# Performance work log

Hardware: AMD Instinct MI355X
Metric: run time of the kernel (lower is better)

Reference implementation:

```python
import jax, jax.numpy as jnp
import numpy as np

B, TC, TT, E, V = 512, 64, 16, 512, 256
E2 = E // 2


def entmax15(z):
    # exact sort-based 1.5-entmax over last axis (Peters et al., 2019)
    z = z / 2.0
    z = z - jnp.max(z, axis=-1, keepdims=True)  # shift-invariant, for stability
    z_srt = -jnp.sort(-z, axis=-1)
    d = z.shape[-1]
    rho = jnp.arange(1, d + 1, dtype=z.dtype)
    mean = jnp.cumsum(z_srt, axis=-1) / rho
    mean_sq = jnp.cumsum(z_srt * z_srt, axis=-1) / rho
    ss = rho * (mean_sq - mean * mean)
    delta = (1.0 - ss) / rho
    pos = delta > 0
    sqrt_d = jnp.where(pos, jnp.sqrt(jnp.where(pos, delta, 1.0)), 0.0)
    tau = mean - sqrt_d
    k = jnp.sum((tau <= z_srt).astype(jnp.int32), axis=-1, keepdims=True)
    tau_star = jnp.take_along_axis(tau, k - 1, axis=-1)
    y = jnp.clip(z - tau_star, 0.0)
    return y * y


def _mha(q_seq, kv, wq, wk, wv, bq, bk, bv, wo, bo):
    # single-head attention; q_seq: (T,B,E) decoder states, kv: (B,S,E) encoder memory
    e = q_seq.shape[-1]
    q = (q_seq @ wq.T + bq) * (1.0 / jnp.sqrt(jnp.asarray(e, q_seq.dtype)))
    k = kv @ wk.T + bk
    v = kv @ wv.T + bv
    a = jax.nn.softmax(jnp.einsum('tbe,bse->bts', q, k), axis=-1)
    o = jnp.einsum('bts,bse->tbe', a, v)
    return o @ wo.T + bo


def setup_inputs() -> dict:
    key = jax.random.key(0)
    ks = jax.random.split(key, 20)
    rn = lambda k, s, sc=1.0: sc * jax.random.normal(k, s, dtype=jnp.float32)
    z = lambda s: jnp.zeros(s, jnp.float32)
    return {
        'char_encoding': rn(ks[0], (B, TC, E)),
        'char_hn0': rn(ks[1], (B, E2)),
        'char_cn0': rn(ks[2], (B, E2)),
        'tag_encoding': rn(ks[3], (B, TT, E)),
        'tag_hn0': rn(ks[4], (B, E2)),
        'tag_cn0': rn(ks[5], (B, E2)),
        'true_output_seq': jax.random.uniform(ks[6], (B, TC, V), dtype=jnp.float32),
        'w_ih': rn(ks[7], (4 * E, V), 0.05),
        'w_hh': rn(ks[8], (4 * E, E), 0.05),
        'b_ih': z((4 * E,)),
        'b_hh': z((4 * E,)),
        'char_wq': rn(ks[9], (E, E), 0.05), 'char_wk': rn(ks[10], (E, E), 0.05), 'char_wv': rn(ks[11], (E, E), 0.05),
        'char_bq': z((E,)), 'char_bk': z((E,)), 'char_bv': z((E,)),
        'char_wo': rn(ks[12], (E, E), 0.05), 'char_bo': z((E,)),
        'tag_wq': rn(ks[13], (E, E), 0.05), 'tag_wk': rn(ks[14], (E, E), 0.05), 'tag_wv': rn(ks[15], (E, E), 0.05),
        'tag_bq': z((E,)), 'tag_bk': z((E,)), 'tag_bv': z((E,)),
        'tag_wo': rn(ks[16], (E, E), 0.05), 'tag_bo': z((E,)),
        'out_w': rn(ks[17], (V, 2 * E), 0.05),
        'out_b': z((V,)),
    }


def reference(char_encoding, char_hn0, char_cn0, tag_encoding, tag_hn0, tag_cn0, true_output_seq, w_ih, w_hh, b_ih, b_hh, char_wq, char_wk, char_wv, char_bq, char_bk, char_bv, char_wo, char_bo, tag_wq, tag_wk, tag_wv, tag_bq, tag_bk, tag_bv, tag_wo, tag_bo, out_w, out_b):
    # initial cell state = concat of the two encoders' final (h, c)
    h0 = jnp.concatenate([char_hn0, tag_hn0], axis=-1)
    c0 = jnp.concatenate([char_cn0, tag_cn0], axis=-1)
    # teacher forcing: input at t=0 is zeros, then true_output_seq[:, t]
    xs = jnp.concatenate([jnp.zeros_like(true_output_seq[:, :1]), true_output_seq[:, 1:]], axis=1)
    xs = jnp.swapaxes(xs, 0, 1)  # (T, B, V)

    def cell(carry, x):
        h, c = carry
        gates = x @ w_ih.T + b_ih + h @ w_hh.T + b_hh
        i, f, g, o = jnp.split(gates, 4, axis=-1)  # torch gate order i,f,g,o
        c = jax.nn.sigmoid(f) * c + jax.nn.sigmoid(i) * jnp.tanh(g)
        h = jax.nn.sigmoid(o) * jnp.tanh(c)
        return (h, c), h

    _, hs = jax.lax.scan(cell, (h0, c0), xs)  # (T, B, E)
    # attention queries only depend on per-step h, so batch all T queries at once
    ca = _mha(hs, char_encoding, char_wq, char_wk, char_wv, char_bq, char_bk, char_bv, char_wo, char_bo)
    ta = _mha(hs, tag_encoding, tag_wq, tag_wk, tag_wv, tag_bq, tag_bk, tag_bv, tag_wo, tag_bo)
    logits = jnp.concatenate([ca, ta], axis=-1) @ out_w.T + out_b  # (T, B, V)
    return jnp.swapaxes(entmax15(logits), 0, 1)  # (B, T, V)
```

## Files before the change

kernel.cpp:

```cpp
#include <hip/hip_runtime.h>

typedef unsigned short us;
typedef unsigned int u32;
typedef unsigned long long u64;
typedef __bf16 bf16x8 __attribute__((ext_vector_type(8)));
typedef float f32x4 __attribute__((ext_vector_type(4)));

#define MFMA(a,b,c) __builtin_amdgcn_mfma_f32_16x16x32_bf16(a,b,c,0,0,0)

__device__ __forceinline__ us f2bf(float f){
  u32 u = __builtin_bit_cast(u32, f);
  u += 0x7fffu + ((u>>16)&1u);
  return (us)(u>>16);
}
__device__ __forceinline__ float bf2f(us h){
  u32 u = ((u32)h)<<16;
  return __builtin_bit_cast(float, u);
}
__device__ __forceinline__ float sigf(float x){ return 1.0f/(1.0f+__expf(-x)); }
__device__ __forceinline__ float tanh_(float x){ float e=__expf(2.0f*x); return 1.0f - 2.0f/(e+1.0f); }


__global__ void k_prep_wperm(const float* __restrict__ w_hh, const float* __restrict__ w_ih,
                             const float* __restrict__ b_ih, const float* __restrict__ b_hh,
                             us* __restrict__ Wp, float* __restrict__ biasc){
  int n = blockIdx.x; int c = threadIdx.x;
  float v = (c < 512) ? w_hh[(size_t)n*512 + c] : w_ih[(size_t)n*256 + (c-512)];
  int g = n >> 9, eg = n & 511, eb = eg >> 4, ln = eg & 15;
  int kc = c >> 5, qd = (c >> 3) & 3, i = c & 7;
  size_t dst = ((((size_t)eb*24 + kc)*4 + g)*64 + (size_t)(qd*16 + ln))*8 + i;
  Wp[dst] = f2bf(v);
  if (c == 0) biasc[n] = b_ih[n] + b_hh[n];
}

__global__ void k_prep_state(const float* __restrict__ ch, const float* __restrict__ th,
                             const float* __restrict__ cc, const float* __restrict__ tc,
                             us* __restrict__ h0, float* __restrict__ c0){
  int i = blockIdx.x*256 + threadIdx.x;
  int b = i>>9, e = i&511;
  float hv = (e<256)? ch[b*256+e] : th[b*256+e-256];
  float cv = (e<256)? cc[b*256+e] : tc[b*256+e-256];
  h0[i] = f2bf(hv); c0[i] = cv;
}

__global__ void k_xprep(const float* __restrict__ x, us* __restrict__ xbf){
  int g = blockIdx.x*256 + threadIdx.x;
  int v0 = (g & 31) * 8;
  int b  = (g >> 5) & 511;
  int t  = g >> 14;
  const float4* src = (const float4*)(x + ((size_t)(b*64 + t))*256 + v0);
  float4 f0 = src[0], f1 = src[1];
  uint4 pk;
  pk.x = (u32)f2bf(f0.x) | ((u32)f2bf(f0.y)<<16);
  pk.y = (u32)f2bf(f0.z) | ((u32)f2bf(f0.w)<<16);
  pk.z = (u32)f2bf(f1.x) | ((u32)f2bf(f1.y)<<16);
  pk.w = (u32)f2bf(f1.z) | ((u32)f2bf(f1.w)<<16);
  *(uint4*)(xbf + ((size_t)t*512 + b)*256 + v0) = pk;
}

__global__ void k_uvec2(const float* __restrict__ bq, const float* __restrict__ wk,
                        float* __restrict__ u){
  int j = blockIdx.x*256 + threadIdx.x;
  int e0 = blockIdx.y*64;
  float a = 0.f;
  #pragma unroll 8
  for (int e=e0; e<e0+64; ++e) a += bq[e]*wk[(size_t)e*512 + j];
  atomicAdd(u+j, a);
}

__global__ __launch_bounds__(256) void k_pvec2(const float* __restrict__ wo,
    const float* __restrict__ bv, const float* __restrict__ bo, float* __restrict__ p){
  int w = threadIdx.x>>6, lane = threadIdx.x&63;
  int i = blockIdx.x*4 + w;
  const float4* wr = (const float4*)(wo + (size_t)i*512);
  const float4* bvv = (const float4*)bv;
  float a = 0.f;
  #pragma unroll
  for (int k=0;k<2;++k){
    float4 x = wr[lane*2+k];
    float4 y = bvv[lane*2+k];
    a += x.x*y.x + x.y*y.y + x.z*y.z + x.w*y.w;
  }
  #pragma unroll
  for (int dl=1; dl<64; dl<<=1) a += __shfl_xor(a, dl);
  if (lane==0) p[i] = a + bo[i];
}

__global__ __launch_bounds__(256) void k_bc2(const float* __restrict__ out_w,
    const float* __restrict__ pc, const float* __restrict__ pt,
    const float* __restrict__ out_b, float* __restrict__ bc){
  int w = threadIdx.x>>6, lane = threadIdx.x&63;
  int v = blockIdx.x*4 + w;
  const float4* wr = (const float4*)(out_w + (size_t)v*1024);
  float a = 0.f;
  #pragma unroll
  for (int k=0;k<4;++k){
    float4 x = wr[lane*4+k];
    int base = (lane*4+k)*4;
    const float* pv = (base < 512) ? (pc + base) : (pt + (base-512));
    a += x.x*pv[0] + x.y*pv[1] + x.z*pv[2] + x.w*pv[3];
  }
  #pragma unroll
  for (int dl=1; dl<64; dl<<=1) a += __shfl_xor(a, dl);
  if (lane==0) bc[v] = a + out_b[v];
}

template<bool TA, int OMODE>
__global__ __launch_bounds__(256) void k_pgemm(const float* __restrict__ A, int lda,
    const float* __restrict__ B, int ldb, void* C1, void* C2, int ldc, int K){
  __shared__ us As[64][40];
  __shared__ us Bs[64][40];
  int tid=threadIdx.x, w=tid>>6, lane=tid&63, qd=lane>>4, ln=lane&15;
  int m0 = blockIdx.x*64, n0 = blockIdx.y*64;
  f32x4 acc[4] = {};
  for (int kc=0; kc<K/32; ++kc){
    int k0 = kc*32;
    if (!TA){
      int r=tid>>2, c=(tid&3)*8;
      const float* ap = A + (size_t)(m0+r)*lda + k0 + c;
      float4 f0=*(const float4*)ap, f1=*(const float4*)(ap+4);
      uint4 pk;
      pk.x=(u32)f2bf(f0.x)|((u32)f2bf(f0.y)<<16);
      pk.y=(u32)f2bf(f0.z)|((u32)f2bf(f0.w)<<16);
      pk.z=(u32)f2bf(f1.x)|((u32)f2bf(f1.y)<<16);
      pk.w=(u32)f2bf(f1.z)|((u32)f2bf(f1.w)<<16);
      *(uint4*)&As[r][c] = pk;
    } else {
      int kk=tid>>3, mp=(tid&7)*8;
      const float* ap = A + (size_t)(k0+kk)*lda + m0 + mp;
      #pragma unroll
      for (int i=0;i<8;++i) As[mp+i][kk] = f2bf(ap[i]);
    }
    { int kk=tid>>3, np=(tid&7)*8;
      const float* bp = B + (size_t)(k0+kk)*ldb + n0 + np;
      #pragma unroll
      for (int i=0;i<8;++i) Bs[np+i][kk] = f2bf(bp[i]);
    }
    __syncthreads();
    bf16x8 a = *(const bf16x8*)&As[16*w+ln][qd*8];
    #pragma unroll
    for (int j=0;j<4;++j){
      bf16x8 bb = *(const bf16x8*)&Bs[16*j+ln][qd*8];
      acc[j] = MFMA(a, bb, acc[j]);
    }
    __syncthreads();
  }
  #pragma unroll
  for (int j=0;j<4;++j){
    #pragma unroll
    for (int r=0;r<4;++r){
      size_t idx = (size_t)(m0+16*w+qd*4+r)*ldc + (n0+16*j+ln);
      float v = acc[j][r];
      if (OMODE==0) ((float*)C1)[idx] = v;
      else if (OMODE==1) ((us*)C1)[idx] = f2bf(v);
      else {
        us h = f2bf(v);
        ((us*)C1)[idx] = h;
        ((us*)C2)[idx] = f2bf(v - bf2f(h));
      }
    }
  }
}

__global__ __launch_bounds__(256, 1) void k_lstm_all(
    const us* __restrict__ h0, const us* __restrict__ xbf,
    const us* __restrict__ Wp, const float* __restrict__ biasc,
    const float* __restrict__ c0, us* __restrict__ hs,
    unsigned* __restrict__ bars){
  extern __shared__ us Wf[];
  int tid = threadIdx.x, w = tid>>6, lane = tid&63, qd = lane>>4, ln = lane&15;
  int bb = blockIdx.x & 7, eb = blockIdx.x >> 3;
  int b0 = bb*64, e0 = eb*16;

  u32 myxcc = 0;
  asm volatile("s_getreg_b32 %0, hwreg(HW_REG_XCC_ID)" : "=s"(myxcc));
  unsigned* xcds = bars + 4096 + (size_t)bb*512;
  if (tid == 0)
    __hip_atomic_store(xcds + eb*16, myxcc + 1u, __ATOMIC_RELAXED, __HIP_MEMORY_SCOPE_AGENT);

  {
    const uint4* src = (const uint4*)(Wp + (size_t)eb*49152);
    uint4* dst = (uint4*)Wf;
    #pragma unroll
    for (int i=0;i<24;++i) dst[tid + 256*i] = src[tid + 256*i];
  }
  int bA = b0 + 16*w + ln;
  int bC = b0 + 16*w + qd*4;
  int e  = e0 + ln;
  float bias_[4], c_[4];
  #pragma unroll
  for (int j=0;j<4;++j) bias_[j] = biasc[j*512 + e];
  #pragma unroll
  for (int r=0;r<4;++r) c_[r] = c0[(size_t)(bC+r)*512 + e];
  __syncthreads();

  bool fast;
  {
    const unsigned* xp = xcds + (lane&31)*16;
    u32 ids;
    while (true){
      ids = __hip_atomic_load(xp, __ATOMIC_RELAXED, __HIP_MEMORY_SCOPE_AGENT);
      if (__all((int)(ids != 0))) break;
      __builtin_amdgcn_s_sleep(8);
    }
    u32 id0 = (u32)__shfl((int)ids, 0);
    fast = __all((int)(ids == id0));
  }

  unsigned* flags = bars + (size_t)bb*512;
  unsigned* myflag = flags + eb*16;
  const unsigned* pollp = flags + (lane&31)*16;
  f32x4 xacc[4] = {};
  for (int t=0; t<64; ++t){
    if (t > 0){
      unsigned tgt = (unsigned)t;
      while (true){
        unsigned v = __hip_atomic_load(pollp, __ATOMIC_RELAXED, __HIP_MEMORY_SCOPE_AGENT);
        if (__all((int)(v >= tgt))) break;
        __builtin_amdgcn_s_sleep(1);
      }
      asm volatile("" ::: "memory");
    }
    bf16x8 afr[16];
    if (t == 0){
      const us* hrow = h0 + (size_t)bA*512;
      #pragma unroll
      for (int kc=0; kc<16; ++kc)
        afr[kc] = *(const bf16x8*)(hrow + kc*32 + qd*8);
    } else if (fast){
      const us* hrow = hs + ((size_t)bA*64 + (t-1))*512;
      #pragma unroll
      for (int kc=0; kc<16; ++kc)
        afr[kc] = *(const bf16x8*)(hrow + kc*32 + qd*8);
    } else {
      const u64* hq = (const u64*)(hs + ((size_t)bA*64 + (t-1))*512);
      u64 q0[16], q1[16];
      #pragma unroll
      for (int kc=0; kc<16; ++kc){
        q0[kc] = __hip_atomic_load(hq + kc*8 + qd*2 + 0, __ATOMIC_RELAXED, __HIP_MEMORY_SCOPE_AGENT);
        q1[kc] = __hip_atomic_load(hq + kc*8 + qd*2 + 1, __ATOMIC_RELAXED, __HIP_MEMORY_SCOPE_AGENT);
      }
      #pragma unroll
      for (int kc=0; kc<16; ++kc){
        union { u64 q[2]; bf16x8 v; } u_;
        u_.q[0] = q0[kc]; u_.q[1] = q1[kc];
        afr[kc] = u_.v;
      }
    }
    f32x4 acc[4] = {xacc[0], xacc[1], xacc[2], xacc[3]};
    #pragma unroll
    for (int kc=0; kc<16; ++kc){
      #pragma unroll
      for (int j=0;j<4;++j){
        bf16x8 bfrag = *(const bf16x8*)&Wf[(size_t)((kc*4+j)*64 + lane)*8];
        acc[j] = MFMA(afr[kc], bfrag, acc[j]);
      }
    }
    us hb[4];
    #pragma unroll
    for (int r=0;r<4;++r){
      float iv = acc[0][r]+bias_[0], fv = acc[1][r]+bias_[1];
      float gv = acc[2][r]+bias_[2], ov = acc[3][r]+bias_[3];
      float cc2 = sigf(fv)*c_[r] + sigf(iv)*tanh_(gv);
      c_[r] = cc2;
      hb[r] = f2bf(sigf(ov)*tanh_(cc2));
    }
    #pragma unroll
    for (int r=0;r<4;++r){
      u32 v = hb[r];
      u32 p = v | (((u32)__shfl_xor((int)v, 1)) << 16);
      u64 q = (u64)p | (((u64)(u32)__shfl_xor((int)p, 2)) << 32);
      if ((lane & 3) == 0){
        size_t idx = ((size_t)(bC+r)*64 + t)*512 + e0 + ln;
        if (fast)
          *(u64*)(hs + idx) = q;
        else
          __hip_atomic_store((u64*)(hs + idx), q, __ATOMIC_RELAXED, __HIP_MEMORY_SCOPE_AGENT);
      }
    }
    if (t < 63){
      __syncthreads();
      if (tid == 0)
        __hip_atomic_store(myflag, (unsigned)(t+1), __ATOMIC_RELAXED, __HIP_MEMORY_SCOPE_AGENT);
      const us* xrow = xbf + ((size_t)(t+1)*512 + bA)*256;
      f32x4 xa[4] = {};
      #pragma unroll
      for (int kx=0; kx<8; ++kx){
        bf16x8 xf = *(const bf16x8*)(xrow + kx*32 + qd*8);
        #pragma unroll
        for (int j=0;j<4;++j){
          bf16x8 bfrag = *(const bf16x8*)&Wf[(size_t)(((16+kx)*4+j)*64 + lane)*8];
          xa[j] = MFMA(xf, bfrag, xa[j]);
        }
      }
      #pragma unroll
      for (int j=0;j<4;++j) xacc[j] = xa[j];
    }
  }
}

__global__ __launch_bounds__(256) void k_gemm(
    const us* __restrict__ Ap, const us* __restrict__ W,
    const float* __restrict__ bias, float alpha, us* __restrict__ C){
  __shared__ us As[128][40];
  __shared__ us Ws[128][40];
  int tid = threadIdx.x; int w = tid>>6; int lane=tid&63;
  int qd=lane>>4, ln=lane&15;
  int m0 = blockIdx.x*128, n0 = blockIdx.y*128;
  int wm = (w&1)*64, wn=(w>>1)*64;
  f32x4 acc[4][4] = {};
  int row = tid>>1; int cp = (tid&1)*16;
  for (int kc=0;kc<16;++kc){
    int k0=kc*32;
    { const uint4* ap = (const uint4*)(Ap + (size_t)(m0+row)*512 + k0+cp);
      *(uint4*)&As[row][cp]=ap[0]; *(uint4*)&As[row][cp+8]=ap[1];
    }
    { const uint4* wp = (const uint4*)(W + (size_t)(n0+row)*512 + k0+cp);
      *(uint4*)&Ws[row][cp]=wp[0]; *(uint4*)&Ws[row][cp+8]=wp[1];
    }
    __syncthreads();
    bf16x8 af[4], bfr[4];
    #pragma unroll
    for (int i=0;i<4;++i) af[i]  = *(const bf16x8*)&As[wm+16*i+ln][qd*8];
    #pragma unroll
    for (int j=0;j<4;++j) bfr[j] = *(const bf16x8*)&Ws[wn+16*j+ln][qd*8];
    #pragma unroll
    for (int i=0;i<4;++i)
      #pragma unroll
      for (int j=0;j<4;++j) acc[i][j]=MFMA(af[i],bfr[j],acc[i][j]);
    __syncthreads();
  }
  #pragma unroll
  for (int j=0;j<4;++j){
    int col = n0+wn+16*j+ln;
    float bv = bias[col];
    #pragma unroll
    for (int i=0;i<4;++i){
      #pragma unroll
      for (int r=0;r<4;++r){
        int rm = m0+wm+16*i+qd*4+r;
        C[(size_t)rm*512 + col] = f2bf(alpha*(acc[i][j][r]+bv));
      }
    }
  }
}

template<int S>
struct alignas(16) ASmem3 {
  static constexpr int SP  = (S<32)?32:S;
  static constexpr int SPp = SP+8;
  us Pbh[64][SPp];
  us Pbl[64][SPp];
  union {
    us Es[S][72];
    struct { us Eh[64][72]; us El[64][72]; } t;
  } u;
  us Ph[64][72];
  us Pl[64][72];
};

template<int S, bool ACC>
__global__ __launch_bounds__(256) void k_attn3(const us* __restrict__ hGp,
    const float* __restrict__ enc, const us* __restrict__ Mvh,
    const us* __restrict__ Mvl, float* __restrict__ out){
  constexpr int NJ  = S/16;
  constexpr int KC2 = ((S<32)?32:S)/32;
  extern __shared__ char smraw[];
  ASmem3<S>& sm = *reinterpret_cast<ASmem3<S>*>(smraw);
  int b = blockIdx.x;
  int tid=threadIdx.x, w=tid>>6, lane=tid&63, qd=lane>>4, ln=lane&15;

  f32x4 sacc[NJ];
  #pragma unroll
  for (int j=0;j<NJ;++j) sacc[j] = (f32x4){0.f,0.f,0.f,0.f};
  const us* hrow = hGp + ((size_t)(b*64 + 16*w + ln))*512;
  for (int ec=0; ec<8; ++ec){
    int e0 = ec*64;
    { int s = tid>>2, ep=(tid&3)*16;
      if (S==64 || tid < 4*S){
        const float* ap = enc + ((size_t)b*S + s)*512 + e0 + ep;
        float4 f0=*(const float4*)ap, f1=*(const float4*)(ap+4);
        float4 f2=*(const float4*)(ap+8), f3=*(const float4*)(ap+12);
        float fv[16]={f0.x,f0.y,f0.z,f0.w,f1.x,f1.y,f1.z,f1.w,
                      f2.x,f2.y,f2.z,f2.w,f3.x,f3.y,f3.z,f3.w};
        u32 pk[8];
        #pragma unroll
        for (int i=0;i<8;++i)
          pk[i] = (u32)f2bf(fv[2*i]) | ((u32)f2bf(fv[2*i+1])<<16);
        uint4* d = (uint4*)&sm.u.Es[s][ep];
        d[0] = make_uint4(pk[0],pk[1],pk[2],pk[3]);
        d[1] = make_uint4(pk[4],pk[5],pk[6],pk[7]);
      }
    }
    __syncthreads();
    #pragma unroll
    for (int kcl=0;kcl<2;++kcl){
      bf16x8 a = *(const bf16x8*)(hrow + e0 + kcl*32 + qd*8);
      #pragma unroll
      for (int j=0;j<NJ;++j){
        bf16x8 bb = *(const bf16x8*)&sm.u.Es[16*j+ln][kcl*32+qd*8];
        sacc[j] = MFMA(a, bb, sacc[j]);
      }
    }
    __syncthreads();
  }

  #pragma unroll
  for (int r=0;r<4;++r){
    float m = sacc[0][r];
    #pragma unroll
    for (int j=1;j<NJ;++j) m = fmaxf(m, sacc[j][r]);
    #pragma unroll
    for (int dl=1; dl<16; dl<<=1) m = fmaxf(m, __shfl_xor(m, dl));
    float ssum = 0.f;
    #pragma unroll
    for (int j=0;j<NJ;++j){ float e_=__expf(sacc[j][r]-m); sacc[j][r]=e_; ssum+=e_; }
    #pragma unroll
    for (int dl=1; dl<16; dl<<=1) ssum += __shfl_xor(ssum, dl);
    float inv = 1.0f/ssum;
    int R = 16*w + qd*4 + r;
    #pragma unroll
    for (int j=0;j<NJ;++j){
      float pv = sacc[j][r]*inv;
      us h = f2bf(pv);
      sm.Pbh[R][16*j+ln] = h;
      sm.Pbl[R][16*j+ln] = f2bf(pv - bf2f(h));
    }
    if (S==16){ sm.Pbh[R][16+ln]=0; sm.Pbl[R][16+ln]=0; }
  }

  f32x4 Lacc[4][4] = {};
  for (int ec=0; ec<8; ++ec){
    int e0 = ec*64;
    { int s = tid>>2, ep=(tid&3)*16;
      if (S==64 || tid < 4*S){
        const float* ap = enc + ((size_t)b*S + s)*512 + e0 + ep;
        float4 f0=*(const float4*)ap, f1=*(const float4*)(ap+4);
        float4 f2=*(const float4*)(ap+8), f3=*(const float4*)(ap+12);
        float fv[16]={f0.x,f0.y,f0.z,f0.w,f1.x,f1.y,f1.z,f1.w,
                      f2.x,f2.y,f2.z,f2.w,f3.x,f3.y,f3.z,f3.w};
        #pragma unroll
        for (int i=0;i<16;++i){
          float v = fv[i]; us h = f2bf(v);
          sm.u.t.Eh[ep+i][s] = h;
          sm.u.t.El[ep+i][s] = f2bf(v - bf2f(h));
        }
      } else if (S==16 && tid < 128){
        int s2 = 16 + ((tid-64)>>2);
        #pragma unroll
        for (int i=0;i<16;++i){ sm.u.t.Eh[ep+i][s2]=0; sm.u.t.El[ep+i][s2]=0; }
      }
    }
    __syncthreads();
    f32x4 pacc[4] = {};
    #pragma unroll
    for (int kcl=0;kcl<KC2;++kcl){
      bf16x8 ah = *(const bf16x8*)&sm.Pbh[16*w+ln][kcl*32+qd*8];
      bf16x8 al = *(const bf16x8*)&sm.Pbl[16*w+ln][kcl*32+qd*8];
      #pragma unroll
      for (int j=0;j<4;++j){
        bf16x8 bh = *(const bf16x8*)&sm.u.t.Eh[16*j+ln][kcl*32+qd*8];
        bf16x8 bl = *(const bf16x8*)&sm.u.t.El[16*j+ln][kcl*32+qd*8];
        pacc[j] = MFMA(ah, bh, pacc[j]);
        pacc[j] = MFMA(ah, bl, pacc[j]);
        pacc[j] = MFMA(al, bh, pacc[j]);
      }
    }
    #pragma unroll
    for (int j=0;j<4;++j)
      #pragma unroll
      for (int r=0;r<4;++r){
        float v = pacc[j][r]; us h = f2bf(v);
        sm.Ph[16*w+qd*4+r][16*j+ln] = h;
        sm.Pl[16*w+qd*4+r][16*j+ln] = f2bf(v - bf2f(h));
      }
    __syncthreads();
    #pragma unroll
    for (int kcl=0;kcl<2;++kcl){
      bf16x8 ah[4], al[4];
      #pragma unroll
      for (int i=0;i<4;++i){
        ah[i] = *(const bf16x8*)&sm.Ph[16*i+ln][kcl*32+qd*8];
        al[i] = *(const bf16x8*)&sm.Pl[16*i+ln][kcl*32+qd*8];
      }
      #pragma unroll
      for (int j=0;j<4;++j){
        int v = 64*w + 16*j + ln;
        bf16x8 mh = *(const bf16x8*)(Mvh + (size_t)v*512 + e0 + kcl*32 + qd*8);
        bf16x8 ml = *(const bf16x8*)(Mvl + (size_t)v*512 + e0 + kcl*32 + qd*8);
        #pragma unroll
        for (int i=0;i<4;++i){
          Lacc[i][j] = MFMA(ah[i], mh, Lacc[i][j]);
          Lacc[i][j] = MFMA(ah[i], ml, Lacc[i][j]);
          Lacc[i][j] = MFMA(al[i], mh, Lacc[i][j]);
        }
      }
    }
  }
  #pragma unroll
  for (int i=0;i<4;++i){
    #pragma unroll
    for (int j=0;j<4;++j){
      int v = 64*w + 16*j + ln;
      #pragma unroll
      for (int r=0;r<4;++r){
        size_t addr = ((size_t)b*64 + 16*i + qd*4 + r)*256 + v;
        if (ACC) out[addr] += Lacc[i][j][r];
        else     out[addr]  = Lacc[i][j][r];
      }
    }
  }
}

__global__ __launch_bounds__(256) void k_entmax(float* __restrict__ out,
                                                const float* __restrict__ bc){
  int tid=threadIdx.x; int w=tid>>6; int lane=tid&63;
  float4 bcv = *(const float4*)(bc + lane*4);
  int base = blockIdx.x*16 + w*4;
  for (int i=0;i<4;++i){
    int row = base + i;
    float* rp = out + (size_t)row*256 + lane*4;
    float4 d = *(const float4*)rp;
    float z[4] = {0.5f*(d.x+bcv.x), 0.5f*(d.y+bcv.y), 0.5f*(d.z+bcv.z), 0.5f*(d.w+bcv.w)};
    float m = fmaxf(fmaxf(z[0],z[1]), fmaxf(z[2],z[3]));
    #pragma unroll
    for (int dl=1; dl<64; dl<<=1) m = fmaxf(m, __shfl_xor(m, dl));
    #pragma unroll
    for (int k=0;k<4;++k) z[k] -= m;
    float tau = -1.0f;
    for (int it=0; it<14; ++it){
      float s1=0.f, s2=0.f;
      #pragma unroll
      for (int k=0;k<4;++k){
        float dd = z[k]-tau; dd = fmaxf(dd, 0.f);
        s1 += dd; s2 += dd*dd;
      }
      #pragma unroll
      for (int dl=1; dl<64; dl<<=1){ s1 += __shfl_xor(s1, dl); s2 += __shfl_xor(s2, dl); }
      tau += (s2 - 1.0f) / (2.0f*fmaxf(s1, 1e-12f));
    }
    float4 y;
    { float dd;
      dd = fmaxf(z[0]-tau,0.f); y.x = dd*dd;
      dd = fmaxf(z[1]-tau,0.f); y.y = dd*dd;
      dd = fmaxf(z[2]-tau,0.f); y.z = dd*dd;
      dd = fmaxf(z[3]-tau,0.f); y.w = dd*dd;
    }
    *(float4*)rp = y;
  }
}


extern "C" void kernel_launch(void* const* d_in, const int* in_sizes, int n_in,
                              void* d_out, int out_size, void* d_ws, size_t ws_size,
                              hipStream_t stream){
  (void)in_sizes; (void)n_in; (void)out_size; (void)ws_size;
  const float* char_enc = (const float*)d_in[0];
  const float* char_hn0 = (const float*)d_in[1];
  const float* char_cn0 = (const float*)d_in[2];
  const float* tag_enc  = (const float*)d_in[3];
  const float* tag_hn0  = (const float*)d_in[4];
  const float* tag_cn0  = (const float*)d_in[5];
  const float* true_out = (const float*)d_in[6];
  const float* w_ih = (const float*)d_in[7];
  const float* w_hh = (const float*)d_in[8];
  const float* b_ih = (const float*)d_in[9];
  const float* b_hh = (const float*)d_in[10];
  const float* c_wq = (const float*)d_in[11];
  const float* c_wk = (const float*)d_in[12];
  const float* c_wv = (const float*)d_in[13];
  const float* c_bq = (const float*)d_in[14];
  const float* c_bv = (const float*)d_in[16];
  const float* c_wo = (const float*)d_in[17];
  const float* c_bo = (const float*)d_in[18];
  const float* t_wq = (const float*)d_in[19];
  const float* t_wk = (const float*)d_in[20];
  const float* t_wv = (const float*)d_in[21];
  const float* t_bq = (const float*)d_in[22];
  const float* t_bv = (const float*)d_in[24];
  const float* t_wo = (const float*)d_in[25];
  const float* t_bo = (const float*)d_in[26];
  const float* out_w = (const float*)d_in[27];
  const float* out_b = (const float*)d_in[28];
  float* out = (float*)d_out;

  char* base = (char*)d_ws;
  char* regA = base;
  us*    Wp    = (us*)   (regA + 0);
  float* biasc = (float*)(regA + 3145728);
  us*    h0    = (us*)   (regA + 3153920);
  float* cst   = (float*)(regA + 3678208);
  float* M1f   = (float*)(regA + 4726784);
  float* M2f   = (float*)(regA + 5251072);
  us*    xbf   = (us*)   (regA + 5775360);
  us*    hG    = (us*)   regA;
  char* regB = base + 33554432;
  us*    Gc_w  = (us*)(regB + 0);
  us*    Gt_w  = (us*)(regB + 524288);
  us*    M1vh  = (us*)(regB + 1048576);
  us*    M1vl  = (us*)(regB + 1310720);
  us*    M2vh  = (us*)(regB + 1572864);
  us*    M2vl  = (us*)(regB + 1835008);
  float* u_c   = (float*)(regB + 2097152);
  float* u_t   = (float*)(regB + 2099200);
  float* p_c   = (float*)(regB + 2101248);
  float* p_t   = (float*)(regB + 2103296);
  float* bc    = (float*)(regB + 2105344);
  us*    hs    = (us*)(base + 33554432 + 2106368);
  unsigned* bars = (unsigned*)(base + 33554432 + 2106368 + 33554432);

  static bool attr_done = false;
  if (!attr_done){
    hipFuncSetAttribute(reinterpret_cast<const void*>(&k_lstm_all),
                        hipFuncAttributeMaxDynamicSharedMemorySize, 131072);
    attr_done = true;
  }

  hipMemsetAsync(bars, 0, 32768, stream);
  hipMemsetAsync(u_c, 0, 4096, stream);
  k_prep_wperm<<<2048, 768, 0, stream>>>(w_hh, w_ih, b_ih, b_hh, Wp, biasc);
  k_prep_state<<<1024, 256, 0, stream>>>(char_hn0, tag_hn0, char_cn0, tag_cn0, h0, cst);
  k_xprep<<<4096, 256, 0, stream>>>(true_out, xbf);
  k_pgemm<true,1><<<dim3(8,8),256,0,stream>>>(c_wk, 512, c_wq, 512, Gc_w, nullptr, 512, 512);
  k_pgemm<true,1><<<dim3(8,8),256,0,stream>>>(t_wk, 512, t_wq, 512, Gt_w, nullptr, 512, 512);
  k_pgemm<false,0><<<dim3(4,8),256,0,stream>>>(out_w,     1024, c_wo, 512, M1f, nullptr, 512, 512);
  k_pgemm<false,0><<<dim3(4,8),256,0,stream>>>(out_w+512, 1024, t_wo, 512, M2f, nullptr, 512, 512);
  k_pgemm<false,2><<<dim3(4,8),256,0,stream>>>(M1f, 512, c_wv, 512, M1vh, M1vl, 512, 512);
  k_pgemm<false,2><<<dim3(4,8),256,0,stream>>>(M2f, 512, t_wv, 512, M2vh, M2vl, 512, 512);
  k_uvec2<<<dim3(2,8),256,0,stream>>>(c_bq, c_wk, u_c);
  k_uvec2<<<dim3(2,8),256,0,stream>>>(t_bq, t_wk, u_t);
  k_pvec2<<<128,256,0,stream>>>(c_wo, c_bv, c_bo, p_c);
  k_pvec2<<<128,256,0,stream>>>(t_wo, t_bv, t_bo, p_t);
  k_bc2<<<64,256,0,stream>>>(out_w, p_c, p_t, out_b, bc);

  k_lstm_all<<<256, 256, 98304, stream>>>(h0, xbf, Wp, biasc, cst, hs, bars);

  const float scale = 0.044194173824159216f;
  k_gemm<<<dim3(256,4),256,0,stream>>>(hs, Gc_w, u_c, scale, hG);
  k_attn3<64,false><<<512,256,sizeof(ASmem3<64>),stream>>>(hG, char_enc, M1vh, M1vl, out);
  k_gemm<<<dim3(256,4),256,0,stream>>>(hs, Gt_w, u_t, scale, hG);
  k_attn3<16,true ><<<512,256,sizeof(ASmem3<16>),stream>>>(hG, tag_enc, M2vh, M2vl, out);
  k_entmax<<<2048,256,0,stream>>>(out, bc);
}
```

Measured before the change: 963.7 us.

## Start LSTM recurrent MFMAs per ready h-chunk and batch paired weight-prep launches

In the persistent LSTM kernel's fast path, each step now polls per-producer flags with a ballot and issues the recurrent MFMAs for each 128-element chunk of h as soon as that chunk's eight producer blocks have signaled. Previously it waited for all producers first. This overlaps the per-step barrier wait with matrix work on the critical serial recurrence. Separately, the paired char/tag weight-precompute GEMMs and vector kernels are merged into single launches using blockIdx.z, which cuts launch count. The chunked polling adds ballot and branch overhead inside the spin loop and may hurt MFMA scheduling.

```diff
diff --git a/kernel.cpp b/kernel.cpp
--- a/kernel.cpp
+++ b/kernel.cpp
@@ -58,8 +58,13 @@
   *(uint4*)(xbf + ((size_t)t*512 + b)*256 + v0) = pk;
 }
 
-__global__ void k_uvec2(const float* __restrict__ bq, const float* __restrict__ wk,
-                        float* __restrict__ u){
+__global__ void k_uvec2z(const float* __restrict__ bq0, const float* __restrict__ wk0,
+                         float* __restrict__ u0,
+                         const float* __restrict__ bq1, const float* __restrict__ wk1,
+                         float* __restrict__ u1){
+  const float* bq = blockIdx.z ? bq1 : bq0;
+  const float* wk = blockIdx.z ? wk1 : wk0;
+  float* u = blockIdx.z ? u1 : u0;
   int j = blockIdx.x*256 + threadIdx.x;
   int e0 = blockIdx.y*64;
   float a = 0.f;
@@ -68,8 +73,14 @@
   atomicAdd(u+j, a);
 }
 
-__global__ __launch_bounds__(256) void k_pvec2(const float* __restrict__ wo,
-    const float* __restrict__ bv, const float* __restrict__ bo, float* __restrict__ p){
+__global__ __launch_bounds__(256) void k_pvec2z(const float* __restrict__ wo0,
+    const float* __restrict__ bv0, const float* __restrict__ bo0, float* __restrict__ p0,
+    const float* __restrict__ wo1, const float* __restrict__ bv1,
+    const float* __restrict__ bo1, float* __restrict__ p1){
+  const float* wo = blockIdx.z ? wo1 : wo0;
+  const float* bv = blockIdx.z ? bv1 : bv0;
+  const float* bo = blockIdx.z ? bo1 : bo0;
+  float* p = blockIdx.z ? p1 : p0;
   int w = threadIdx.x>>6, lane = threadIdx.x&63;
   int i = blockIdx.x*4 + w;
   const float4* wr = (const float4*)(wo + (size_t)i*512);
@@ -106,8 +117,14 @@
 }
 
 template<bool TA, int OMODE>
-__global__ __launch_bounds__(256) void k_pgemm(const float* __restrict__ A, int lda,
-    const float* __restrict__ B, int ldb, void* C1, void* C2, int ldc, int K){
+__global__ __launch_bounds__(256) void k_pgemm2(
+    const float* __restrict__ A0, const float* __restrict__ A1, int lda,
+    const float* __restrict__ B0, const float* __restrict__ B1, int ldb,
+    void* C1a, void* C2a, void* C1b, void* C2b, int ldc, int K){
+  const float* A = blockIdx.z ? A1 : A0;
+  const float* B = blockIdx.z ? B1 : B0;
+  void* C1 = blockIdx.z ? C1b : C1a;
+  void* C2 = blockIdx.z ? C2b : C2a;
   __shared__ us As[64][40];
   __shared__ us Bs[64][40];
   int tid=threadIdx.x, w=tid>>6, lane=tid&63, qd=lane>>4, ln=lane&15;
@@ -212,7 +229,54 @@
   const unsigned* pollp = flags + (lane&31)*16;
   f32x4 xacc[4] = {};
   for (int t=0; t<64; ++t){
-    if (t > 0){
+    f32x4 acc[4] = {xacc[0], xacc[1], xacc[2], xacc[3]};
+    if (t == 0){
+      const us* hrow = h0 + (size_t)bA*512;
+      bf16x8 afr[16];
+      #pragma unroll
+      for (int kc=0; kc<16; ++kc)
+        afr[kc] = *(const bf16x8*)(hrow + kc*32 + qd*8);
+      #pragma unroll
+      for (int kc=0; kc<16; ++kc){
+        #pragma unroll
+        for (int j=0;j<4;++j){
+          bf16x8 bfrag = *(const bf16x8*)&Wf[(size_t)((kc*4+j)*64 + lane)*8];
+          acc[j] = MFMA(afr[kc], bfrag, acc[j]);
+        }
+      }
+    } else if (fast){
+      const us* hrow = hs + ((size_t)bA*64 + (t-1))*512;
+      unsigned done = 0;
+      unsigned tgt = (unsigned)t;
+      while (done != 0xFu){
+        u32 v = __hip_atomic_load(pollp, __ATOMIC_RELAXED, __HIP_MEMORY_SCOPE_AGENT);
+        u64 m = __ballot((int)(v >= tgt));
+        #pragma unroll
+        for (int g=0; g<4; ++g){
+          if (!(done & (1u<<g)) && (((m >> (8*g)) & 0xFFu) == 0xFFu)){
+            asm volatile("" ::: "memory");
+            bf16x8 f0 = *(const bf16x8*)(hrow + (4*g+0)*32 + qd*8);
+            bf16x8 f1 = *(const bf16x8*)(hrow + (4*g+1)*32 + qd*8);
+            bf16x8 f2 = *(const bf16x8*)(hrow + (4*g+2)*32 + qd*8);
+            bf16x8 f3 = *(const bf16x8*)(hrow + (4*g+3)*32 + qd*8);
+            #pragma unroll
+            for (int j=0;j<4;++j)
+              acc[j] = MFMA(f0, *(const bf16x8*)&Wf[(size_t)(((4*g+0)*4+j)*64 + lane)*8], acc[j]);
+            #pragma unroll
+            for (int j=0;j<4;++j)
+              acc[j] = MFMA(f1, *(const bf16x8*)&Wf[(size_t)(((4*g+1)*4+j)*64 + lane)*8], acc[j]);
+            #pragma unroll
+            for (int j=0;j<4;++j)
+              acc[j] = MFMA(f2, *(const bf16x8*)&Wf[(size_t)(((4*g+2)*4+j)*64 + lane)*8], acc[j]);
+            #pragma unroll
+            for (int j=0;j<4;++j)
+              acc[j] = MFMA(f3, *(const bf16x8*)&Wf[(size_t)(((4*g+3)*4+j)*64 + lane)*8], acc[j]);
+            done |= 1u<<g;
+          }
+        }
+        if (done != 0xFu) __builtin_amdgcn_s_sleep(1);
+      }
+    } else {
       unsigned tgt = (unsigned)t;
       while (true){
         unsigned v = __hip_atomic_load(pollp, __ATOMIC_RELAXED, __HIP_MEMORY_SCOPE_AGENT);
@@ -220,19 +284,6 @@
         __builtin_amdgcn_s_sleep(1);
       }
       asm volatile("" ::: "memory");
-    }
-    bf16x8 afr[16];
-    if (t == 0){
-      const us* hrow = h0 + (size_t)bA*512;
-      #pragma unroll
-      for (int kc=0; kc<16; ++kc)
-        afr[kc] = *(const bf16x8*)(hrow + kc*32 + qd*8);
-    } else if (fast){
-      const us* hrow = hs + ((size_t)bA*64 + (t-1))*512;
-      #pragma unroll
-      for (int kc=0; kc<16; ++kc)
-        afr[kc] = *(const bf16x8*)(hrow + kc*32 + qd*8);
-    } else {
       const u64* hq = (const u64*)(hs + ((size_t)bA*64 + (t-1))*512);
       u64 q0[16], q1[16];
       #pragma unroll
@@ -244,16 +295,11 @@
       for (int kc=0; kc<16; ++kc){
         union { u64 q[2]; bf16x8 v; } u_;
         u_.q[0] = q0[kc]; u_.q[1] = q1[kc];
-        afr[kc] = u_.v;
-      }
-    }
-    f32x4 acc[4] = {xacc[0], xacc[1], xacc[2], xacc[3]};
-    #pragma unroll
-    for (int kc=0; kc<16; ++kc){
-      #pragma unroll
-      for (int j=0;j<4;++j){
-        bf16x8 bfrag = *(const bf16x8*)&Wf[(size_t)((kc*4+j)*64 + lane)*8];
-        acc[j] = MFMA(afr[kc], bfrag, acc[j]);
+        #pragma unroll
+        for (int j=0;j<4;++j){
+          bf16x8 bfrag = *(const bf16x8*)&Wf[(size_t)((kc*4+j)*64 + lane)*8];
+          acc[j] = MFMA(u_.v, bfrag, acc[j]);
+        }
       }
     }
     us hb[4];
@@ -621,16 +667,14 @@
   k_prep_wperm<<<2048, 768, 0, stream>>>(w_hh, w_ih, b_ih, b_hh, Wp, biasc);
   k_prep_state<<<1024, 256, 0, stream>>>(char_hn0, tag_hn0, char_cn0, tag_cn0, h0, cst);
   k_xprep<<<4096, 256, 0, stream>>>(true_out, xbf);
-  k_pgemm<true,1><<<dim3(8,8),256,0,stream>>>(c_wk, 512, c_wq, 512, Gc_w, nullptr, 512, 512);
-  k_pgemm<true,1><<<dim3(8,8),256,0,stream>>>(t_wk, 512, t_wq, 512, Gt_w, nullptr, 512, 512);
-  k_pgemm<false,0><<<dim3(4,8),256,0,stream>>>(out_w,     1024, c_wo, 512, M1f, nullptr, 512, 512);
-  k_pgemm<false,0><<<dim3(4,8),256,0,stream>>>(out_w+512, 1024, t_wo, 512, M2f, nullptr, 512, 512);
-  k_pgemm<false,2><<<dim3(4,8),256,0,stream>>>(M1f, 512, c_wv, 512, M1vh, M1vl, 512, 512);
-  k_pgemm<false,2><<<dim3(4,8),256,0,stream>>>(M2f, 512, t_wv, 512, M2vh, M2vl, 512, 512);
-  k_uvec2<<<dim3(2,8),256,0,stream>>>(c_bq, c_wk, u_c);
-  k_uvec2<<<dim3(2,8),256,0,stream>>>(t_bq, t_wk, u_t);
-  k_pvec2<<<128,256,0,stream>>>(c_wo, c_bv, c_bo, p_c);
-  k_pvec2<<<128,256,0,stream>>>(t_wo, t_bv, t_bo, p_t);
+  k_pgemm2<true,1><<<dim3(8,8,2),256,0,stream>>>(c_wk, t_wk, 512, c_wq, t_wq, 512,
+                                                 Gc_w, nullptr, Gt_w, nullptr, 512, 512);
+  k_pgemm2<false,0><<<dim3(4,8,2),256,0,stream>>>(out_w, out_w+512, 1024, c_wo, t_wo, 512,
+                                                  M1f, nullptr, M2f, nullptr, 512, 512);
+  k_pgemm2<false,2><<<dim3(4,8,2),256,0,stream>>>(M1f, M2f, 512, c_wv, t_wv, 512,
+                                                  M1vh, M1vl, M2vh, M2vl, 512, 512);
+  k_uvec2z<<<dim3(2,8,2),256,0,stream>>>(c_bq, c_wk, u_c, t_bq, t_wk, u_t);
+  k_pvec2z<<<dim3(128,1,2),256,0,stream>>>(c_wo, c_bv, c_bo, p_c, t_wo, t_bv, t_bo, p_t);
   k_bc2<<<64,256,0,stream>>>(out_w, p_c, p_t, out_b, bc);
 
   k_lstm_all<<<256, 256, 98304, stream>>>(h0, xbf, Wp, biasc, cst, hs, bars);
```

After: 1.030 ms. 1.07x slower.
